# Performance work log

Hardware: AMD Instinct MI355X
Metric: run time of the kernel (lower is better)

Reference implementation:

```python
import jax, jax.numpy as jnp
import numpy as np

N_ENTITY = 100000
N_RELATION = 32
DIM = 64
N_LAYER = 2
B = 4096
T = 32


def _knowledge_attention(h_set, path, t_emb, W1, W2):
    # h_set, path, t_emb: [B, T, D]
    x = jnp.concatenate([h_set, path], axis=-1)          # [B, T, 2D]
    a = jax.nn.sigmoid(jax.nn.sigmoid(x @ W1) @ W2)      # [B, T]
    w = jax.nn.softmax(a, axis=-1)                       # softmax over triples
    return jnp.einsum('bt,btd->bd', w, t_emb)            # [B, D]


def _branch(h_idx, r_idx, t_idx, ent, rel, W1, W2):
    # h_idx/r_idx/t_idx: [L, B, T] ints. Faithful to the original loop,
    # which re-adds layer-i head emb and re-multiplies layer-i relation emb i times.
    outs = []
    for i in range(N_LAYER):
        h_set = ent[h_idx[0]]                            # [B, T, D]
        path = rel[r_idx[0]]                             # [B, T, D]
        for _k in range(1, i + 1):
            h_set = h_set + ent[h_idx[i]]
            path = path * rel[r_idx[i]]
        outs.append(_knowledge_attention(h_set, path, ent[t_idx[i]], W1, W2))
    return outs


def setup_inputs() -> dict:
    key = jax.random.key(0)
    ks = jax.random.split(key, 20)
    d = {}
    d['items'] = jax.random.randint(ks[0], (B,), 0, N_ENTITY)
    names = ['uis', 'ipt', 'upt', 'iot']
    i = 1
    for nm in names:
        d[nm + '_h'] = jax.random.randint(ks[i], (N_LAYER, B, T), 0, N_ENTITY); i += 1
        d[nm + '_r'] = jax.random.randint(ks[i], (N_LAYER, B, T), 0, N_RELATION); i += 1
        d[nm + '_t'] = jax.random.randint(ks[i], (N_LAYER, B, T), 0, N_ENTITY); i += 1
    # xavier-ish scales
    d['ent_emb'] = jax.random.normal(ks[13], (N_ENTITY, DIM), jnp.float32) * 0.05
    d['rel_emb'] = jax.random.normal(ks[14], (N_RELATION, DIM), jnp.float32) * 0.05
    d['W1'] = jax.random.normal(ks[15], (2 * DIM, DIM), jnp.float32) * (1.0 / np.sqrt(2 * DIM))
    d['W2'] = jax.random.normal(ks[16], (DIM,), jnp.float32) * (1.0 / np.sqrt(DIM))
    return d


def reference(items, uis_h, uis_r, uis_t, ipt_h, ipt_r, ipt_t,
              upt_h, upt_r, upt_t, iot_h, iot_r, iot_t,
              ent_emb, rel_emb, W1, W2):
    # user embeddings (init triple set)
    user_embs = [ent_emb[uis_h[0]].mean(axis=1)]
    user_embs += _branch(uis_h, uis_r, uis_t, ent_emb, rel_emb, W1, W2)
    # item embeddings (potential triple set)
    item_embs = [ent_emb[items]]
    item_embs += _branch(ipt_h, ipt_r, ipt_t, ent_emb, rel_emb, W1, W2)
    # user potential embeddings
    upo_embs = [ent_emb[upt_h[0]].mean(axis=1)]
    upo_embs += _branch(upt_h, upt_r, upt_t, ent_emb, rel_emb, W1, W2)
    # item origin embeddings
    ior_embs = [ent_emb[iot_h[0]].mean(axis=1)]
    ior_embs += _branch(iot_h, iot_r, iot_t, ent_emb, rel_emb, W1, W2)
    # agg == 'sum': extra item term appended before predict
    item_embs.append(ent_emb[ipt_h[0]].mean(axis=1))
    e_u = sum(user_embs[1:], user_embs[0])
    e_i = sum(item_embs[1:], item_embs[0])
    e_p_u = sum(upo_embs[1:], upo_embs[0])
    e_p_i = sum(ior_embs[1:], ior_embs[0])
    e_u = jnp.concatenate([e_u, e_p_u], axis=-1)
    e_i = jnp.concatenate([e_p_i, e_i], axis=-1)
    scores = jax.nn.sigmoid((e_i * e_u).sum(axis=1))     # [B]
    kge_loss = jnp.float32(0.0)                          # agg='sum' path: no SSL loss
    return scores, kge_loss
```

## Files before the change

kernel.cpp:

```cpp
#include <hip/hip_runtime.h>


#define NE   100000
#define NR   32
#define DIMD 64
#define BB   4096
#define TT   32
#define BT   (BB * TT)

__device__ __forceinline__ float sigf(float x) { return 1.0f / (1.0f + __expf(-x)); }
__device__ __forceinline__ float4 ld4(const float* p) {
    return *reinterpret_cast<const float4*>(p);
}

__global__ __launch_bounds__(256) void k_proj_ent(const float* __restrict__ ent,
                                                  const float* __restrict__ W1,
                                                  float* __restrict__ Pent) {
    __shared__ float sW[64][68];
    __shared__ float sR[64][68];
    const int tid = threadIdx.x;
    const int row0 = blockIdx.x * 64;

#pragma unroll
    for (int i = 0; i < 4; ++i) {
        const int idx = tid + 256 * i;
        const int r = idx >> 4;
        const int c = idx & 15;
        const float4 wv = ld4(W1 + r * DIMD + 4 * c);
        sW[r][4 * c + 0] = wv.x; sW[r][4 * c + 1] = wv.y;
        sW[r][4 * c + 2] = wv.z; sW[r][4 * c + 3] = wv.w;
        const int er = (row0 + r < NE) ? (row0 + r) : (NE - 1);
        const float4 rv = ld4(ent + er * DIMD + 4 * c);
        sR[r][4 * c + 0] = rv.x; sR[r][4 * c + 1] = rv.y;
        sR[r][4 * c + 2] = rv.z; sR[r][4 * c + 3] = rv.w;
    }
    __syncthreads();

    const int q = tid & 15;
    const int trow = tid >> 4;
    float4 acc0 = make_float4(0.f, 0.f, 0.f, 0.f);
    float4 acc1 = acc0, acc2 = acc0, acc3 = acc0;

#pragma unroll
    for (int kk = 0; kk < 16; ++kk) {
        const float4 r0 = ld4(&sR[4 * trow + 0][4 * kk]);
        const float4 r1 = ld4(&sR[4 * trow + 1][4 * kk]);
        const float4 r2 = ld4(&sR[4 * trow + 2][4 * kk]);
        const float4 r3 = ld4(&sR[4 * trow + 3][4 * kk]);
#pragma unroll
        for (int i = 0; i < 4; ++i) {
            const float4 wv = ld4(&sW[4 * kk + i][4 * q]);
            const float s0 = (i == 0) ? r0.x : (i == 1) ? r0.y : (i == 2) ? r0.z : r0.w;
            const float s1 = (i == 0) ? r1.x : (i == 1) ? r1.y : (i == 2) ? r1.z : r1.w;
            const float s2 = (i == 0) ? r2.x : (i == 1) ? r2.y : (i == 2) ? r2.z : r2.w;
            const float s3 = (i == 0) ? r3.x : (i == 1) ? r3.y : (i == 2) ? r3.z : r3.w;
            acc0.x = fmaf(s0, wv.x, acc0.x); acc0.y = fmaf(s0, wv.y, acc0.y);
            acc0.z = fmaf(s0, wv.z, acc0.z); acc0.w = fmaf(s0, wv.w, acc0.w);
            acc1.x = fmaf(s1, wv.x, acc1.x); acc1.y = fmaf(s1, wv.y, acc1.y);
            acc1.z = fmaf(s1, wv.z, acc1.z); acc1.w = fmaf(s1, wv.w, acc1.w);
            acc2.x = fmaf(s2, wv.x, acc2.x); acc2.y = fmaf(s2, wv.y, acc2.y);
            acc2.z = fmaf(s2, wv.z, acc2.z); acc2.w = fmaf(s2, wv.w, acc2.w);
            acc3.x = fmaf(s3, wv.x, acc3.x); acc3.y = fmaf(s3, wv.y, acc3.y);
            acc3.z = fmaf(s3, wv.z, acc3.z); acc3.w = fmaf(s3, wv.w, acc3.w);
        }
    }

    const int orow = row0 + 4 * trow;
    if (orow + 0 < NE) *reinterpret_cast<float4*>(Pent + (orow + 0) * DIMD + 4 * q) = acc0;
    if (orow + 1 < NE) *reinterpret_cast<float4*>(Pent + (orow + 1) * DIMD + 4 * q) = acc1;
    if (orow + 2 < NE) *reinterpret_cast<float4*>(Pent + (orow + 2) * DIMD + 4 * q) = acc2;
    if (orow + 3 < NE) *reinterpret_cast<float4*>(Pent + (orow + 3) * DIMD + 4 * q) = acc3;
}

__global__ __launch_bounds__(256) void k_proj_rel(const float* __restrict__ rel,
                                                  const float* __restrict__ W1,
                                                  float* __restrict__ Prel1,
                                                  float* __restrict__ Prel2) {
    int gid = blockIdx.x * 256 + threadIdx.x;
    int row = gid >> 6;
    int d = gid & 63;
    if (row < 1024) {
        const float* a = rel + (row >> 5) * DIMD;
        const float* c = rel + (row & 31) * DIMD;
        float acc = 0.0f;
#pragma unroll
        for (int k = 0; k < DIMD; ++k)
            acc = fmaf(a[k] * c[k], W1[(DIMD + k) * DIMD + d], acc);
        Prel2[row * DIMD + d] = acc;
    } else if (row < 1056) {
        const float* a = rel + (row - 1024) * DIMD;
        float acc = 0.0f;
#pragma unroll
        for (int k = 0; k < DIMD; ++k)
            acc = fmaf(a[k], W1[(DIMD + k) * DIMD + d], acc);
        Prel1[(row - 1024) * DIMD + d] = acc;
    }
}

__global__ __launch_bounds__(256) void k_main(
    const int* __restrict__ items,
    const int* __restrict__ uh, const int* __restrict__ ur, const int* __restrict__ ut,
    const int* __restrict__ ih, const int* __restrict__ ir, const int* __restrict__ itp,
    const int* __restrict__ ph, const int* __restrict__ pr, const int* __restrict__ pt,
    const int* __restrict__ oh, const int* __restrict__ orr, const int* __restrict__ ot,
    const float* __restrict__ ent, const float* __restrict__ W2,
    const float* __restrict__ Pent, const float* __restrict__ Prel1,
    const float* __restrict__ Prel2, float* __restrict__ out) {
    const int b = blockIdx.x;
    const int tid = threadIdx.x;
    const int w = tid >> 6;
    const int lane = tid & 63;
    const int g = lane >> 4;
    const int q = lane & 15;

    const int* hp;
    const int* rp;
    const int* tp;
    switch (w) {
        case 0: hp = uh; rp = ur; tp = ut; break;
        case 1: hp = ih; rp = ir; tp = itp; break;
        case 2: hp = ph; rp = pr; tp = pt; break;
        default: hp = oh; rp = orr; tp = ot; break;
    }

    __shared__ int sidx[4][3][2][TT];
    {
        const int l = lane >> 5;
        const int t0 = lane & 31;
        const int off = l * BT + b * TT + t0;
        sidx[w][0][l][t0] = hp[off];
        sidx[w][1][l][t0] = rp[off];
        sidx[w][2][l][t0] = tp[off];
    }
    const int item_idx = (w == 1) ? items[b] : 0;

    const float4 w2v = ld4(W2 + 4 * q);

    float a0[8], a1[8];
    float4 accH = make_float4(0.f, 0.f, 0.f, 0.f);
#pragma unroll
    for (int p = 0; p < 8; ++p) {
        const int t = 4 * p + g;
        const int ih0 = sidx[w][0][0][t];
        const int ih1 = sidx[w][0][1][t];
        const int ir0 = sidx[w][1][0][t];
        const int ir1 = sidx[w][1][1][t];
        const float* pA0 = Pent + (ih0 << 6) + 4 * q;
        const float* pA1 = Pent + (ih1 << 6) + 4 * q;
        const float* pR0 = Prel1 + (ir0 << 6) + 4 * q;
        const float* pR2 = Prel2 + ((ir0 * 32 + ir1) << 6) + 4 * q;
        const float* pH = ent + (ih0 << 6) + 4 * q;
        const float4 A0 = ld4(pA0);
        const float4 A1 = ld4(pA1);
        const float4 R0 = ld4(pR0);
        const float4 R2 = ld4(pR2);
        const float4 H = ld4(pH);

        accH.x += H.x; accH.y += H.y; accH.z += H.z; accH.w += H.w;

        float d0 = sigf(A0.x + R0.x) * w2v.x;
        d0 = fmaf(sigf(A0.y + R0.y), w2v.y, d0);
        d0 = fmaf(sigf(A0.z + R0.z), w2v.z, d0);
        d0 = fmaf(sigf(A0.w + R0.w), w2v.w, d0);

        float d1 = sigf(A0.x + A1.x + R2.x) * w2v.x;
        d1 = fmaf(sigf(A0.y + A1.y + R2.y), w2v.y, d1);
        d1 = fmaf(sigf(A0.z + A1.z + R2.z), w2v.z, d1);
        d1 = fmaf(sigf(A0.w + A1.w + R2.w), w2v.w, d1);

#pragma unroll
        for (int m = 1; m < 16; m <<= 1) {
            d0 += __shfl_xor(d0, m, 64);
            d1 += __shfl_xor(d1, m, 64);
        }
        a0[p] = sigf(d0);
        a1[p] = sigf(d1);
    }

    float s0 = 0.0f, s1 = 0.0f;
#pragma unroll
    for (int p = 0; p < 8; ++p) {
        a0[p] = __expf(a0[p]); s0 += a0[p];
        a1[p] = __expf(a1[p]); s1 += a1[p];
    }
    s0 += __shfl_xor(s0, 16, 64);
    s0 += __shfl_xor(s0, 32, 64);
    s1 += __shfl_xor(s1, 16, 64);
    s1 += __shfl_xor(s1, 32, 64);
    const float inv0 = 1.0f / s0;
    const float inv1 = 1.0f / s1;

    float4 acc = make_float4(0.03125f * accH.x, 0.03125f * accH.y,
                             0.03125f * accH.z, 0.03125f * accH.w);
#pragma unroll
    for (int p = 0; p < 8; ++p) {
        const int t = 4 * p + g;
        const int it0 = sidx[w][2][0][t];
        const int it1 = sidx[w][2][1][t];
        const float* pT0 = ent + (it0 << 6) + 4 * q;
        const float* pT1 = ent + (it1 << 6) + 4 * q;
        const float4 T0 = ld4(pT0);
        const float4 T1 = ld4(pT1);
        const float w0 = a0[p] * inv0;
        const float w1 = a1[p] * inv1;
        acc.x = fmaf(w0, T0.x, fmaf(w1, T1.x, acc.x));
        acc.y = fmaf(w0, T0.y, fmaf(w1, T1.y, acc.y));
        acc.z = fmaf(w0, T0.z, fmaf(w1, T1.z, acc.z));
        acc.w = fmaf(w0, T0.w, fmaf(w1, T1.w, acc.w));
    }
    acc.x += __shfl_xor(acc.x, 16, 64); acc.x += __shfl_xor(acc.x, 32, 64);
    acc.y += __shfl_xor(acc.y, 16, 64); acc.y += __shfl_xor(acc.y, 32, 64);
    acc.z += __shfl_xor(acc.z, 16, 64); acc.z += __shfl_xor(acc.z, 32, 64);
    acc.w += __shfl_xor(acc.w, 16, 64); acc.w += __shfl_xor(acc.w, 32, 64);

    if (w == 1) {
        const float4 iv = ld4(ent + (item_idx << 6) + 4 * q);
        acc.x += iv.x; acc.y += iv.y; acc.z += iv.z; acc.w += iv.w;
    }

    __shared__ float vec[4][DIMD];
    if (g == 0) {
        vec[w][4 * q + 0] = acc.x;
        vec[w][4 * q + 1] = acc.y;
        vec[w][4 * q + 2] = acc.z;
        vec[w][4 * q + 3] = acc.w;
    }
    __syncthreads();

    if (tid < 64) {
        float z = fmaf(vec[0][tid], vec[3][tid], vec[2][tid] * vec[1][tid]);
#pragma unroll
        for (int m = 1; m < 64; m <<= 1) z += __shfl_xor(z, m, 64);
        if (tid == 0) out[b] = sigf(z);
    }
    if (b == 0 && tid == 0) out[BB] = 0.0f;
}

extern "C" void kernel_launch(void* const* d_in, const int* in_sizes, int n_in,
                              void* d_out, int out_size, void* d_ws, size_t ws_size,
                              hipStream_t stream) {
    const int* items = (const int*)d_in[0];
    const int* uh = (const int*)d_in[1];
    const int* ur = (const int*)d_in[2];
    const int* ut = (const int*)d_in[3];
    const int* ih = (const int*)d_in[4];
    const int* ir = (const int*)d_in[5];
    const int* itp = (const int*)d_in[6];
    const int* ph = (const int*)d_in[7];
    const int* pr = (const int*)d_in[8];
    const int* pt = (const int*)d_in[9];
    const int* oh = (const int*)d_in[10];
    const int* orr = (const int*)d_in[11];
    const int* ot = (const int*)d_in[12];
    const float* ent = (const float*)d_in[13];
    const float* rel = (const float*)d_in[14];
    const float* W1 = (const float*)d_in[15];
    const float* W2 = (const float*)d_in[16];
    float* out = (float*)d_out;

    float* Pent = (float*)d_ws;
    float* Prel1 = Pent + NE * DIMD;
    float* Prel2 = Prel1 + NR * DIMD;

    hipLaunchKernelGGL(k_proj_ent, dim3((NE + 63) / 64), dim3(256), 0,
                       stream, ent, W1, Pent);
    hipLaunchKernelGGL(k_proj_rel, dim3((1056 * 64 + 255) / 256), dim3(256), 0,
                       stream, rel, W1, Prel1, Prel2);
    hipLaunchKernelGGL(k_main, dim3(BB), dim3(256), 0, stream, items, uh, ur, ut,
                       ih, ir, itp, ph, pr, pt, oh, orr, ot, ent, W2, Pent, Prel1,
                       Prel2, out);
}
```

Measured before the change: 227.0 us.

## Interleave entity and projected rows in one table, use DPP reductions

```diff
diff --git a/kernel.cpp b/kernel.cpp
--- a/kernel.cpp
+++ b/kernel.cpp
@@ -13,9 +13,26 @@
     return *reinterpret_cast<const float4*>(p);
 }
 
+template <int CTRL>
+__device__ __forceinline__ float dpp_add(float x) {
+    int r = __builtin_amdgcn_update_dpp(0, __builtin_bit_cast(int, x), CTRL,
+                                        0xf, 0xf, true);
+    return x + __builtin_bit_cast(float, r);
+}
+__device__ __forceinline__ float reduce16(float x) {
+    x = dpp_add<0x121>(x);
+    x = dpp_add<0x122>(x);
+    x = dpp_add<0x124>(x);
+    x = dpp_add<0x128>(x);
+    return x;
+}
+
 __global__ __launch_bounds__(256) void k_proj_ent(const float* __restrict__ ent,
                                                   const float* __restrict__ W1,
-                                                  float* __restrict__ Pent) {
+                                                  float* __restrict__ outP,
+                                                  int pshift,
+                                                  float* __restrict__ outE,
+                                                  int eshift) {
     __shared__ float sW[64][68];
     __shared__ float sR[64][68];
     const int tid = threadIdx.x;
@@ -66,10 +83,16 @@
     }
 
     const int orow = row0 + 4 * trow;
-    if (orow + 0 < NE) *reinterpret_cast<float4*>(Pent + (orow + 0) * DIMD + 4 * q) = acc0;
-    if (orow + 1 < NE) *reinterpret_cast<float4*>(Pent + (orow + 1) * DIMD + 4 * q) = acc1;
-    if (orow + 2 < NE) *reinterpret_cast<float4*>(Pent + (orow + 2) * DIMD + 4 * q) = acc2;
-    if (orow + 3 < NE) *reinterpret_cast<float4*>(Pent + (orow + 3) * DIMD + 4 * q) = acc3;
+#pragma unroll
+    for (int i = 0; i < 4; ++i) {
+        if (orow + i < NE) {
+            const float4 a = (i == 0) ? acc0 : (i == 1) ? acc1 : (i == 2) ? acc2 : acc3;
+            *reinterpret_cast<float4*>(outP + ((size_t)(orow + i) << pshift) + 4 * q) = a;
+            if (outE)
+                *reinterpret_cast<float4*>(outE + ((size_t)(orow + i) << eshift) + 4 * q) =
+                    ld4(&sR[4 * trow + i][4 * q]);
+        }
+    }
 }
 
 __global__ __launch_bounds__(256) void k_proj_rel(const float* __restrict__ rel,
@@ -103,9 +126,11 @@
     const int* __restrict__ ih, const int* __restrict__ ir, const int* __restrict__ itp,
     const int* __restrict__ ph, const int* __restrict__ pr, const int* __restrict__ pt,
     const int* __restrict__ oh, const int* __restrict__ orr, const int* __restrict__ ot,
-    const float* __restrict__ ent, const float* __restrict__ W2,
-    const float* __restrict__ Pent, const float* __restrict__ Prel1,
-    const float* __restrict__ Prel2, float* __restrict__ out) {
+    const float* __restrict__ entT, int eshift,
+    const float* __restrict__ pentT, int pshift,
+    const float* __restrict__ W2,
+    const float* __restrict__ Prel1, const float* __restrict__ Prel2,
+    float* __restrict__ out) {
     const int b = blockIdx.x;
     const int tid = threadIdx.x;
     const int w = tid >> 6;
@@ -136,7 +161,7 @@
 
     const float4 w2v = ld4(W2 + 4 * q);
 
-    float a0[8], a1[8];
+    float d0[8], d1[8];
     float4 accH = make_float4(0.f, 0.f, 0.f, 0.f);
 #pragma unroll
     for (int p = 0; p < 8; ++p) {
@@ -145,85 +170,80 @@
         const int ih1 = sidx[w][0][1][t];
         const int ir0 = sidx[w][1][0][t];
         const int ir1 = sidx[w][1][1][t];
-        const float* pA0 = Pent + (ih0 << 6) + 4 * q;
-        const float* pA1 = Pent + (ih1 << 6) + 4 * q;
-        const float* pR0 = Prel1 + (ir0 << 6) + 4 * q;
-        const float* pR2 = Prel2 + ((ir0 * 32 + ir1) << 6) + 4 * q;
-        const float* pH = ent + (ih0 << 6) + 4 * q;
-        const float4 A0 = ld4(pA0);
-        const float4 A1 = ld4(pA1);
-        const float4 R0 = ld4(pR0);
-        const float4 R2 = ld4(pR2);
-        const float4 H = ld4(pH);
+        const float4 A0 = ld4(pentT + ((size_t)ih0 << pshift) + 4 * q);
+        const float4 H  = ld4(entT + ((size_t)ih0 << eshift) + 4 * q);
+        const float4 A1 = ld4(pentT + ((size_t)ih1 << pshift) + 4 * q);
+        const float4 R0 = ld4(Prel1 + (ir0 << 6) + 4 * q);
+        const float4 R2 = ld4(Prel2 + ((ir0 * 32 + ir1) << 6) + 4 * q);
 
         accH.x += H.x; accH.y += H.y; accH.z += H.z; accH.w += H.w;
 
-        float d0 = sigf(A0.x + R0.x) * w2v.x;
-        d0 = fmaf(sigf(A0.y + R0.y), w2v.y, d0);
-        d0 = fmaf(sigf(A0.z + R0.z), w2v.z, d0);
-        d0 = fmaf(sigf(A0.w + R0.w), w2v.w, d0);
-
-        float d1 = sigf(A0.x + A1.x + R2.x) * w2v.x;
-        d1 = fmaf(sigf(A0.y + A1.y + R2.y), w2v.y, d1);
-        d1 = fmaf(sigf(A0.z + A1.z + R2.z), w2v.z, d1);
-        d1 = fmaf(sigf(A0.w + A1.w + R2.w), w2v.w, d1);
-
-#pragma unroll
-        for (int m = 1; m < 16; m <<= 1) {
-            d0 += __shfl_xor(d0, m, 64);
-            d1 += __shfl_xor(d1, m, 64);
-        }
-        a0[p] = sigf(d0);
-        a1[p] = sigf(d1);
-    }
-
+        float v = sigf(A0.x + R0.x) * w2v.x;
+        v = fmaf(sigf(A0.y + R0.y), w2v.y, v);
+        v = fmaf(sigf(A0.z + R0.z), w2v.z, v);
+        v = fmaf(sigf(A0.w + R0.w), w2v.w, v);
+        d0[p] = v;
+
+        float u = sigf(A0.x + A1.x + R2.x) * w2v.x;
+        u = fmaf(sigf(A0.y + A1.y + R2.y), w2v.y, u);
+        u = fmaf(sigf(A0.z + A1.z + R2.z), w2v.z, u);
+        u = fmaf(sigf(A0.w + A1.w + R2.w), w2v.w, u);
+        d1[p] = u;
+    }
+
+    float e0[8], e1[8];
     float s0 = 0.0f, s1 = 0.0f;
 #pragma unroll
     for (int p = 0; p < 8; ++p) {
-        a0[p] = __expf(a0[p]); s0 += a0[p];
-        a1[p] = __expf(a1[p]); s1 += a1[p];
+        e0[p] = __expf(sigf(reduce16(d0[p])));
+        e1[p] = __expf(sigf(reduce16(d1[p])));
+        s0 += e0[p];
+        s1 += e1[p];
     }
     s0 += __shfl_xor(s0, 16, 64);
     s0 += __shfl_xor(s0, 32, 64);
     s1 += __shfl_xor(s1, 16, 64);
     s1 += __shfl_xor(s1, 32, 64);
-    const float inv0 = 1.0f / s0;
-    const float inv1 = 1.0f / s1;
-
-    float4 acc = make_float4(0.03125f * accH.x, 0.03125f * accH.y,
-                             0.03125f * accH.z, 0.03125f * accH.w);
+
+    float4 acc0 = make_float4(0.f, 0.f, 0.f, 0.f);
+    float4 acc1 = acc0;
 #pragma unroll
     for (int p = 0; p < 8; ++p) {
         const int t = 4 * p + g;
         const int it0 = sidx[w][2][0][t];
         const int it1 = sidx[w][2][1][t];
-        const float* pT0 = ent + (it0 << 6) + 4 * q;
-        const float* pT1 = ent + (it1 << 6) + 4 * q;
-        const float4 T0 = ld4(pT0);
-        const float4 T1 = ld4(pT1);
-        const float w0 = a0[p] * inv0;
-        const float w1 = a1[p] * inv1;
-        acc.x = fmaf(w0, T0.x, fmaf(w1, T1.x, acc.x));
-        acc.y = fmaf(w0, T0.y, fmaf(w1, T1.y, acc.y));
-        acc.z = fmaf(w0, T0.z, fmaf(w1, T1.z, acc.z));
-        acc.w = fmaf(w0, T0.w, fmaf(w1, T1.w, acc.w));
-    }
-    acc.x += __shfl_xor(acc.x, 16, 64); acc.x += __shfl_xor(acc.x, 32, 64);
-    acc.y += __shfl_xor(acc.y, 16, 64); acc.y += __shfl_xor(acc.y, 32, 64);
-    acc.z += __shfl_xor(acc.z, 16, 64); acc.z += __shfl_xor(acc.z, 32, 64);
-    acc.w += __shfl_xor(acc.w, 16, 64); acc.w += __shfl_xor(acc.w, 32, 64);
+        const float4 T0 = ld4(entT + ((size_t)it0 << eshift) + 4 * q);
+        const float4 T1 = ld4(entT + ((size_t)it1 << eshift) + 4 * q);
+        acc0.x = fmaf(e0[p], T0.x, acc0.x); acc0.y = fmaf(e0[p], T0.y, acc0.y);
+        acc0.z = fmaf(e0[p], T0.z, acc0.z); acc0.w = fmaf(e0[p], T0.w, acc0.w);
+        acc1.x = fmaf(e1[p], T1.x, acc1.x); acc1.y = fmaf(e1[p], T1.y, acc1.y);
+        acc1.z = fmaf(e1[p], T1.z, acc1.z); acc1.w = fmaf(e1[p], T1.w, acc1.w);
+    }
+
+    const float inv0 = 1.0f / s0;
+    const float inv1 = 1.0f / s1;
+    float4 v;
+    v.x = fmaf(acc0.x, inv0, fmaf(acc1.x, inv1, 0.03125f * accH.x));
+    v.y = fmaf(acc0.y, inv0, fmaf(acc1.y, inv1, 0.03125f * accH.y));
+    v.z = fmaf(acc0.z, inv0, fmaf(acc1.z, inv1, 0.03125f * accH.z));
+    v.w = fmaf(acc0.w, inv0, fmaf(acc1.w, inv1, 0.03125f * accH.w));
+
+    v.x += __shfl_xor(v.x, 16, 64); v.x += __shfl_xor(v.x, 32, 64);
+    v.y += __shfl_xor(v.y, 16, 64); v.y += __shfl_xor(v.y, 32, 64);
+    v.z += __shfl_xor(v.z, 16, 64); v.z += __shfl_xor(v.z, 32, 64);
+    v.w += __shfl_xor(v.w, 16, 64); v.w += __shfl_xor(v.w, 32, 64);
 
     if (w == 1) {
-        const float4 iv = ld4(ent + (item_idx << 6) + 4 * q);
-        acc.x += iv.x; acc.y += iv.y; acc.z += iv.z; acc.w += iv.w;
+        const float4 iv = ld4(entT + ((size_t)item_idx << eshift) + 4 * q);
+        v.x += iv.x; v.y += iv.y; v.z += iv.z; v.w += iv.w;
     }
 
     __shared__ float vec[4][DIMD];
     if (g == 0) {
-        vec[w][4 * q + 0] = acc.x;
-        vec[w][4 * q + 1] = acc.y;
-        vec[w][4 * q + 2] = acc.z;
-        vec[w][4 * q + 3] = acc.w;
+        vec[w][4 * q + 0] = v.x;
+        vec[w][4 * q + 1] = v.y;
+        vec[w][4 * q + 2] = v.z;
+        vec[w][4 * q + 3] = v.w;
     }
     __syncthreads();
 
@@ -258,15 +278,32 @@
     const float* W2 = (const float*)d_in[16];
     float* out = (float*)d_out;
 
-    float* Pent = (float*)d_ws;
-    float* Prel1 = Pent + NE * DIMD;
+    float* Prel1 = (float*)d_ws;
     float* Prel2 = Prel1 + NR * DIMD;
-
-    hipLaunchKernelGGL(k_proj_ent, dim3((NE + 63) / 64), dim3(256), 0,
-                       stream, ent, W1, Pent);
+    float* Ptab = Prel2 + 1024 * DIMD;
+
+    const size_t head = (size_t)(NR * DIMD + 1024 * DIMD) * 4;
+    const size_t need_merged = head + (size_t)NE * 128 * 4;
+    const bool merged = ws_size >= need_merged;
+
+    const float* entT;
+    int eshift;
+    float* pentT;
+    int pshift;
+    if (merged) {
+        entT = Ptab;  eshift = 7;
+        pentT = Ptab + 64; pshift = 7;
+    } else {
+        entT = ent;   eshift = 6;
+        pentT = Ptab; pshift = 6;
+    }
+
+    hipLaunchKernelGGL(k_proj_ent, dim3((NE + 63) / 64), dim3(256), 0, stream,
+                       ent, W1, pentT, pshift, merged ? (float*)entT : nullptr,
+                       eshift);
     hipLaunchKernelGGL(k_proj_rel, dim3((1056 * 64 + 255) / 256), dim3(256), 0,
                        stream, rel, W1, Prel1, Prel2);
     hipLaunchKernelGGL(k_main, dim3(BB), dim3(256), 0, stream, items, uh, ur, ut,
-                       ih, ir, itp, ph, pr, pt, oh, orr, ot, ent, W2, Pent, Prel1,
-                       Prel2, out);
-}
+                       ih, ir, itp, ph, pr, pt, oh, orr, ot, entT, eshift, pentT,
+                       pshift, W2, Prel1, Prel2, out);
+}
```

Measured after the change: 226.8 us. Within noise of the previous version (-0.1%).
